# Kernel optimization log

Hardware: AMD Instinct MI355X
Metric: run time of the kernel (lower is better)

## Reference

```python
import jax, jax.numpy as jnp
import numpy as np

TEMP = 100000.0  # extreme temperature -> softmax ~ hard argmax of nearest past keyframe


def setup_inputs() -> dict:
    key = jax.random.key(0)
    k1, k2, k3 = jax.random.split(key, 3)
    B, T_in, N, T_out = 16, 64, 52, 4096
    root_positions = jax.random.normal(k1, (B, T_in, 3), dtype=jnp.float32)
    joint_rotations_ortho6d = jax.random.normal(k2, (B, T_in, N, 6), dtype=jnp.float32)
    input_frame_indices = jnp.sort(jax.random.randint(k3, (T_in,), 0, T_out, dtype=jnp.int64))
    # guarantee a past keyframe exists for every target (avoids all -inf column / NaN)
    input_frame_indices = input_frame_indices.at[0].set(0)
    target_frame_indices = jnp.arange(T_out, dtype=jnp.int64)
    return {
        "root_positions": root_positions,
        "joint_rotations_ortho6d": joint_rotations_ortho6d,
        "input_frame_indices": input_frame_indices,
        "target_frame_indices": target_frame_indices,
    }


def _zero_velocity(root_positions, joint_rotations_ortho6d,
                   input_frame_indices, target_frame_indices, nb_joints):
    # [T_in, T_out] timestamp differences; future keyframes (diff > 0) masked out
    diff = (input_frame_indices[:, None] - target_frame_indices[None, :]).astype(jnp.float32)
    diff = jnp.where(diff > 0.0, -jnp.inf, diff)
    diff = diff - jnp.max(diff, axis=0, keepdims=True)
    weights = jax.nn.softmax(TEMP * diff, axis=0)  # [T_in, T_out], ~one-hot per column

    # root position: [B, T_in, 3] x [T_in, T_out] -> [B, T_out, 3]
    root = jnp.einsum('btc,ts->bsc', root_positions, weights)
    B, T_out = root.shape[0], root.shape[1]
    # repeat across joints -> [B, T_out, N, 3]
    joint_positions = jnp.broadcast_to(root[:, :, None, :], (B, T_out, nb_joints, 3))
    joint_positions = jnp.asarray(joint_positions)

    # rotations: [B, T_in, N, 6] x [T_in, T_out] -> [B, T_out, N, 6]
    joint_rotations = jnp.einsum('btnc,ts->bsnc', joint_rotations_ortho6d, weights)
    return joint_positions, joint_rotations


def _pad_time(x, t_in):
    # prepend first frame repeated (t_in - 1) times, append last frame once
    front = jnp.repeat(x[:, :1], t_in - 1, axis=1)
    return jnp.concatenate([front, x, x[:, -1:]], axis=1)


def reference(root_positions, joint_rotations_ortho6d,
              input_frame_indices, target_frame_indices):
    nb_joints = joint_rotations_ortho6d.shape[2]
    jp, jr = _zero_velocity(root_positions, joint_rotations_ortho6d,
                            input_frame_indices, target_frame_indices, nb_joints)
    t_in = input_frame_indices.shape[0]
    return _pad_time(jp, t_in), _pad_time(jr, t_in)
```

## Files before the change

### kernel.cpp

```cpp
#include <hip/hip_runtime.h>

constexpr int B     = 16;
constexpr int T_IN  = 64;
constexpr int NJ    = 52;
constexpr int T_OUT = 4096;
constexpr int T_PAD = T_OUT + T_IN;

constexpr int JP_ROW4 = NJ * 3 / 4;
constexpr int JR_ROW4 = NJ * 6 / 4;
constexpr int NROWS   = B * T_PAD;
constexpr int NP4     = NROWS * JP_ROW4;

constexpr int JP_COL4 = B * JP_ROW4;
constexpr int JR_COL4 = B * JR_ROW4;

typedef float f4 __attribute__((ext_vector_type(4)));

__global__ __launch_bounds__(256) void zv_col(
    const float* __restrict__ root,
    const float* __restrict__ rot,
    const int*   __restrict__ idx,
    f4*          __restrict__ out4)
{
    __shared__ int sidx[T_IN];
    __shared__ f4  srm[B];
    const int tid = threadIdx.x;
    if (tid < T_IN) sidx[tid] = idx[tid];
    __syncthreads();

    const int s_out = blockIdx.x;
    int s = s_out - (T_IN - 1);
    s = s < 0 ? 0 : (s > T_OUT - 1 ? T_OUT - 1 : s);

    int ub = 0;
    #pragma unroll
    for (int step = 64; step > 0; step >>= 1)
        if (ub + step <= T_IN && sidx[ub + step - 1] <= s) ub += step;
    const int m = sidx[ub - 1];
    int lo = 0;
    #pragma unroll
    for (int step = 32; step > 0; step >>= 1)
        if (sidx[lo + step - 1] < m) lo += step;
    const int   k   = ub - lo;
    const float inv = 1.0f / (float)k;

    if (tid < B) {
        const float* rp = root + (size_t)(tid * T_IN + lo) * 3;
        float r0 = rp[0], r1 = rp[1], r2 = rp[2];
        for (int q = 1; q < k; ++q) { r0 += rp[3*q]; r1 += rp[3*q+1]; r2 += rp[3*q+2]; }
        f4 v; v.x = r0 * inv; v.y = r1 * inv; v.z = r2 * inv; v.w = 0.f;
        srm[tid] = v;
    }
    __syncthreads();

    for (int f = tid; f < JP_COL4; f += 256) {
        const int b = f / JP_ROW4;
        const int w = f - b * JP_ROW4;
        const f4 rm = srm[b];
        const int md = w % 3;
        const float r0 = rm.x, r1 = rm.y, r2 = rm.z;
        const float x0 = md == 0 ? r0 : (md == 1 ? r1 : r2);
        const float x1 = md == 0 ? r1 : (md == 1 ? r2 : r0);
        const float x2 = md == 0 ? r2 : (md == 1 ? r0 : r1);
        f4 v; v.x = x0; v.y = x1; v.z = x2; v.w = x0;
        out4[(size_t)(b * T_PAD + s_out) * JP_ROW4 + w] = v;
    }

    for (int f = tid; f < JR_COL4; f += 256) {
        const int b = f / JR_ROW4;
        const int w = f - b * JR_ROW4;
        const f4* src = (const f4*)rot + ((size_t)(b * T_IN + lo) * JR_ROW4 + w);
        f4 a = src[0];
        if (k > 1) {
            for (int q = 1; q < k; ++q) a += src[(size_t)q * JR_ROW4];
            a *= inv;
        }
        out4[NP4 + (size_t)(b * T_PAD + s_out) * JR_ROW4 + w] = a;
    }
}

extern "C" void kernel_launch(void* const* d_in, const int* in_sizes, int n_in,
                              void* d_out, int out_size, void* d_ws, size_t ws_size,
                              hipStream_t stream) {
    const float* root = (const float*)d_in[0];
    const float* rot  = (const float*)d_in[1];
    const int*   idx  = (const int*)d_in[2];
    f4* out4 = (f4*)d_out;

    hipLaunchKernelGGL(zv_col, dim3(T_PAD), dim3(256), 0, stream,
                       root, rot, idx, out4);
}
```

Measured before the change: 28.25 us.

## Tile by batch and 32-frame chunk, reuse gathered rotation across runs

Replaces the one-block-per-output-frame grid with blocks that each cover one batch and a 32-frame chunk of output rows. The keyframe search is done per row in shared memory, and each rotation thread walks its rows and reloads the source only when the selected keyframe changes, so repeated rows reuse a register value instead of re-reading global memory. Writes become contiguous within a batch's chunk. Only 234 of 256 threads do rotation work, and each thread's stores stride across rows.

```diff
diff --git a/kernel.cpp b/kernel.cpp
--- a/kernel.cpp
+++ b/kernel.cpp
@@ -11,41 +11,47 @@
 constexpr int NROWS   = B * T_PAD;
 constexpr int NP4     = NROWS * JP_ROW4;
 
-constexpr int JP_COL4 = B * JP_ROW4;
-constexpr int JR_COL4 = B * JR_ROW4;
+constexpr int CHUNK  = 32;
+constexpr int NCHUNK = T_PAD / CHUNK;
 
 typedef float f4 __attribute__((ext_vector_type(4)));
 
-__global__ __launch_bounds__(256) void zv_col(
+__global__ __launch_bounds__(256) void zv_run(
     const float* __restrict__ root,
     const float* __restrict__ rot,
     const int*   __restrict__ idx,
     f4*          __restrict__ out4)
 {
-    __shared__ int sidx[T_IN];
-    __shared__ f4  srm[B];
+    __shared__ int   sidx[T_IN];
+    __shared__ int   ssel[CHUNK];
+    __shared__ float sinv[CHUNK];
+    __shared__ f4    srm[CHUNK];
+
     const int tid = threadIdx.x;
+    const int cs  = blockIdx.x * CHUNK;
+    const int b   = blockIdx.y;
+
     if (tid < T_IN) sidx[tid] = idx[tid];
     __syncthreads();
 
-    const int s_out = blockIdx.x;
-    int s = s_out - (T_IN - 1);
-    s = s < 0 ? 0 : (s > T_OUT - 1 ? T_OUT - 1 : s);
-
-    int ub = 0;
-    #pragma unroll
-    for (int step = 64; step > 0; step >>= 1)
-        if (ub + step <= T_IN && sidx[ub + step - 1] <= s) ub += step;
-    const int m = sidx[ub - 1];
-    int lo = 0;
-    #pragma unroll
-    for (int step = 32; step > 0; step >>= 1)
-        if (sidx[lo + step - 1] < m) lo += step;
-    const int   k   = ub - lo;
-    const float inv = 1.0f / (float)k;
-
-    if (tid < B) {
-        const float* rp = root + (size_t)(tid * T_IN + lo) * 3;
+    if (tid < CHUNK) {
+        const int s_out = cs + tid;
+        int s = s_out - (T_IN - 1);
+        s = s < 0 ? 0 : (s > T_OUT - 1 ? T_OUT - 1 : s);
+        int ub = 0;
+        #pragma unroll
+        for (int st = 64; st > 0; st >>= 1)
+            if (ub + st <= T_IN && sidx[ub + st - 1] <= s) ub += st;
+        const int m = sidx[ub - 1];
+        int lo = 0;
+        #pragma unroll
+        for (int st = 32; st > 0; st >>= 1)
+            if (sidx[lo + st - 1] < m) lo += st;
+        const int   k   = ub - lo;
+        const float inv = 1.0f / (float)k;
+        ssel[tid] = lo | (k << 8);
+        sinv[tid] = inv;
+        const float* rp = root + (size_t)(b * T_IN + lo) * 3;
         float r0 = rp[0], r1 = rp[1], r2 = rp[2];
         for (int q = 1; q < k; ++q) { r0 += rp[3*q]; r1 += rp[3*q+1]; r2 += rp[3*q+2]; }
         f4 v; v.x = r0 * inv; v.y = r1 * inv; v.z = r2 * inv; v.w = 0.f;
@@ -53,29 +59,41 @@
     }
     __syncthreads();
 
-    for (int f = tid; f < JP_COL4; f += 256) {
-        const int b = f / JP_ROW4;
-        const int w = f - b * JP_ROW4;
-        const f4 rm = srm[b];
-        const int md = w % 3;
-        const float r0 = rm.x, r1 = rm.y, r2 = rm.z;
-        const float x0 = md == 0 ? r0 : (md == 1 ? r1 : r2);
-        const float x1 = md == 0 ? r1 : (md == 1 ? r2 : r0);
-        const float x2 = md == 0 ? r2 : (md == 1 ? r0 : r1);
-        f4 v; v.x = x0; v.y = x1; v.z = x2; v.w = x0;
-        out4[(size_t)(b * T_PAD + s_out) * JP_ROW4 + w] = v;
+    {
+        f4* dst = out4 + (size_t)(b * T_PAD + cs) * JP_ROW4;
+        for (int u = tid; u < CHUNK * JP_ROW4; u += 256) {
+            const int r  = u / JP_ROW4;
+            const int md = u % 3;
+            const f4  rm = srm[r];
+            f4 v;
+            v.x = md == 0 ? rm.x : (md == 1 ? rm.y : rm.z);
+            v.y = md == 0 ? rm.y : (md == 1 ? rm.z : rm.x);
+            v.z = md == 0 ? rm.z : (md == 1 ? rm.x : rm.y);
+            v.w = v.x;
+            dst[u] = v;
+        }
     }
 
-    for (int f = tid; f < JR_COL4; f += 256) {
-        const int b = f / JR_ROW4;
-        const int w = f - b * JR_ROW4;
-        const f4* src = (const f4*)rot + ((size_t)(b * T_IN + lo) * JR_ROW4 + w);
-        f4 a = src[0];
-        if (k > 1) {
-            for (int q = 1; q < k; ++q) a += src[(size_t)q * JR_ROW4];
-            a *= inv;
+    if (tid < 234) {
+        const int e = tid % 78;
+        const int j = tid / 78;
+        const f4* rotb = (const f4*)rot + ((size_t)b * T_IN * JR_ROW4 + e);
+        f4*       dst  = out4 + (NP4 + (size_t)(b * T_PAD + cs) * JR_ROW4 + e);
+        int cur = -1;
+        f4  a;
+        for (int r = j; r < CHUNK; r += 3) {
+            const int selr = ssel[r];
+            if (selr != cur) {
+                cur = selr;
+                const int lo = cur & 0xff;
+                const int k  = cur >> 8;
+                const f4* src = rotb + (size_t)lo * JR_ROW4;
+                a = src[0];
+                for (int q = 1; q < k; ++q) a += src[(size_t)q * JR_ROW4];
+                a *= sinv[r];
+            }
+            dst[(size_t)r * JR_ROW4] = a;
         }
-        out4[NP4 + (size_t)(b * T_PAD + s_out) * JR_ROW4 + w] = a;
     }
 }
 
@@ -87,6 +105,6 @@
     const int*   idx  = (const int*)d_in[2];
     f4* out4 = (f4*)d_out;
 
-    hipLaunchKernelGGL(zv_col, dim3(T_PAD), dim3(256), 0, stream,
+    hipLaunchKernelGGL(zv_run, dim3(NCHUNK, B), dim3(256), 0, stream,
                        root, rot, idx, out4);
 }
```

Result: faster. 26.96 us (-4.6%).
